# Kernel optimization log

Measured on AMD Instinct MI355X. Metric: run time of the kernel, lower is better.

Reference implementation:

```python
import jax, jax.numpy as jnp
import numpy as np

TEMPERATURE = 0.5
NEG_FILL = -9e15


def setup_inputs() -> dict:
    key = jax.random.key(0)
    k1, k2 = jax.random.split(key)
    B, D = 8192, 128
    z_i = jax.random.normal(k1, (B, D), dtype=jnp.float32)
    z_j = jax.random.normal(k2, (B, D), dtype=jnp.float32)
    return {"z_i": z_i, "z_j": z_j}


def reference(z_i, z_j):
    B = z_i.shape[0]
    N = 2 * B
    z = jnp.concatenate([z_i, z_j], axis=0)              # [2B, D]
    sim = jnp.matmul(z, z.T) / TEMPERATURE               # [2B, 2B]
    # mask out self-similarity on the diagonal
    diag = jnp.eye(N, dtype=bool)
    sim = jnp.where(diag, NEG_FILL, sim)
    # positive pair of row k is row (k+B) mod 2B
    labels = jnp.concatenate([jnp.arange(B, N), jnp.arange(0, B)])
    # CrossEntropyLoss(reduction='sum'): sum_k logsumexp(sim[k]) - sim[k, labels[k]]
    lse = jax.nn.logsumexp(sim, axis=1)                  # [2B]
    pos = sim[jnp.arange(N), labels]                     # [2B]
    loss = jnp.sum(lse - pos)
    return loss / N
```

## Files before the change

### kernel.cpp

```cpp
#include <hip/hip_runtime.h>

#define TEMP    0.5f
#define LOG2E   1.4426950408889634f
#define C2      (LOG2E / TEMP)
#define MSHIFT  160.0f
#define LN2     0.6931471805599453f
#define NROWS   16384
#define BHALF   8192
#define DDIM    128
#define PREPB   2048

typedef __bf16 bf16x8 __attribute__((ext_vector_type(8)));
typedef float  f32x16 __attribute__((ext_vector_type(16)));

__device__ __forceinline__ float fexp2(float x) {
#if __has_builtin(__builtin_amdgcn_exp2f)
  return __builtin_amdgcn_exp2f(x);
#else
  return exp2f(x);
#endif
}

__device__ __forceinline__ unsigned short f2bf(float f) {
  unsigned int u = __float_as_uint(f);
  unsigned int r = (u + 0x7FFFu + ((u >> 16) & 1u)) >> 16;
  return (unsigned short)r;
}


__global__ void k_prep(const float* __restrict__ zi, const float* __restrict__ zj,
                       unsigned short* __restrict__ zbF,
                       float* __restrict__ S, float* __restrict__ Pp) {
  const int t   = blockIdx.x * 256 + threadIdx.x;
  const int row = t >> 5;
  const int k0  = (t & 31) * 4;
  const float* src = (row < BHALF) ? (zi + (size_t)row * DDIM)
                                   : (zj + (size_t)(row - BHALF) * DDIM);
  float4 v = *reinterpret_cast<const float4*>(src + k0);

  const int g = row >> 5, lo = row & 31, khi = k0 >> 3, j0 = k0 & 7;
  ushort4 o;
  o.x = f2bf(v.x); o.y = f2bf(v.y); o.z = f2bf(v.z); o.w = f2bf(v.w);
  *reinterpret_cast<ushort4*>(zbF + (size_t)g * 4096 + khi * 256 + lo * 8 + j0) = o;

  float dot = 0.f;
  if (row < BHALF) {
    float4 w = *reinterpret_cast<const float4*>(zj + (size_t)row * DDIM + k0);
    dot = fmaf(v.x, w.x, fmaf(v.y, w.y, fmaf(v.z, w.z, v.w * w.w)));
  }
#pragma unroll
  for (int m = 32; m >= 1; m >>= 1) dot += __shfl_xor(dot, m, 64);
  __shared__ float red[4];
  if ((threadIdx.x & 63) == 0) red[threadIdx.x >> 6] = dot;
  __syncthreads();
  if (threadIdx.x == 0) Pp[blockIdx.x] = red[0] + red[1] + red[2] + red[3];

  if (t < NROWS) S[t] = 0.f;
}

template <bool MASK>
__device__ __forceinline__ void expAcc(const f32x16& acc, float& sa, float& sb,
                                       int d, int hi) {
#pragma unroll
  for (int r = 0; r < 16; ++r) {
    float e = fexp2(fmaf(acc[r], C2, -MSHIFT));
    if (MASK) {
      const int rloc = (r & 3) + 8 * (r >> 2) + 4 * hi;
      if (rloc == d) e = 0.f;
    }
    if (r & 1) sb += e; else sa += e;
  }
}

__global__ __launch_bounds__(256, 2)
void k_main(const unsigned short* __restrict__ zbF, float* __restrict__ S) {
  const int wave = threadIdx.x >> 6;
  const int lane = threadIdx.x & 63;
  const int lo = lane & 31;
  const int hi = lane >> 5;
  const int rb = blockIdx.x & 31;
  const int cc = blockIdx.x >> 5;
  const int row0w = rb * 512 + wave * 128;

  bf16x8 b[4][8];
#pragma unroll
  for (int rt = 0; rt < 4; ++rt) {
    const unsigned short* bp = zbF + (size_t)((row0w >> 5) + rt) * 4096 + hi * 256 + lo * 8;
#pragma unroll
    for (int ks = 0; ks < 8; ++ks)
      b[rt][ks] = *reinterpret_cast<const bf16x8*>(bp + ks * 512);
  }

  const f32x16 kZ = {};
  float s[4][2];
#pragma unroll
  for (int rt = 0; rt < 4; ++rt) { s[rt][0] = 0.f; s[rt][1] = 0.f; }

  const int c0base = cc * 1024;
  const unsigned short* abase = zbF + (size_t)(c0base >> 5) * 4096 + hi * 256 + lo * 8;

  bf16x8 a[8];
#pragma unroll
  for (int ks = 0; ks < 8; ++ks)
    a[ks] = *reinterpret_cast<const bf16x8*>(abase + ks * 512);

  for (int it = 0; it < 32; ++it) {
    const int c0 = c0base + it * 32;
    const int dr = c0 - row0w;
    const bool dg = (unsigned)dr < 128u;
    const int rtd = dg ? (dr >> 5) : -1;

    f32x16 acc0 = __builtin_amdgcn_mfma_f32_32x32x16_bf16(a[0], b[0][0], kZ, 0, 0, 0);
    f32x16 acc1 = __builtin_amdgcn_mfma_f32_32x32x16_bf16(a[0], b[1][0], kZ, 0, 0, 0);
#pragma unroll
    for (int ks = 1; ks < 8; ++ks) {
      acc0 = __builtin_amdgcn_mfma_f32_32x32x16_bf16(a[ks], b[0][ks], acc0, 0, 0, 0);
      acc1 = __builtin_amdgcn_mfma_f32_32x32x16_bf16(a[ks], b[1][ks], acc1, 0, 0, 0);
    }
    if (!dg) {
      expAcc<false>(acc0, s[0][0], s[0][1], -1, hi);
      expAcc<false>(acc1, s[1][0], s[1][1], -1, hi);
    } else {
      expAcc<true>(acc0, s[0][0], s[0][1], rtd == 0 ? lo : -1, hi);
      expAcc<true>(acc1, s[1][0], s[1][1], rtd == 1 ? lo : -1, hi);
    }

    acc0 = __builtin_amdgcn_mfma_f32_32x32x16_bf16(a[0], b[2][0], kZ, 0, 0, 0);
    acc1 = __builtin_amdgcn_mfma_f32_32x32x16_bf16(a[0], b[3][0], kZ, 0, 0, 0);
#pragma unroll
    for (int ks = 1; ks < 8; ++ks) {
      acc0 = __builtin_amdgcn_mfma_f32_32x32x16_bf16(a[ks], b[2][ks], acc0, 0, 0, 0);
      acc1 = __builtin_amdgcn_mfma_f32_32x32x16_bf16(a[ks], b[3][ks], acc1, 0, 0, 0);
    }

    if (it + 1 < 32) {
      const unsigned short* ap = abase + (size_t)(it + 1) * 4096;
#pragma unroll
      for (int ks = 0; ks < 8; ++ks)
        a[ks] = *reinterpret_cast<const bf16x8*>(ap + ks * 512);
    }

    if (!dg) {
      expAcc<false>(acc0, s[2][0], s[2][1], -1, hi);
      expAcc<false>(acc1, s[3][0], s[3][1], -1, hi);
    } else {
      expAcc<true>(acc0, s[2][0], s[2][1], rtd == 2 ? lo : -1, hi);
      expAcc<true>(acc1, s[3][0], s[3][1], rtd == 3 ? lo : -1, hi);
    }
  }

#pragma unroll
  for (int rt = 0; rt < 4; ++rt) {
    float v = s[rt][0] + s[rt][1];
    v += __shfl_xor(v, 32, 64);
    if (hi == 0) atomicAdd(&S[row0w + rt * 32 + lo], v);
  }
}

__global__ void k_fin(const float* __restrict__ S, const float* __restrict__ Pp,
                      float* __restrict__ out) {
  const int t = threadIdx.x;
  float q = 0.f;
  for (int r = t; r < NROWS; r += 512)
    q += LN2 * (MSHIFT + __log2f(S[r]));
  for (int r = t; r < PREPB; r += 512)
    q -= 4.0f * Pp[r];
  __shared__ float red[512];
  red[t] = q;
  __syncthreads();
  for (int s2 = 256; s2 > 0; s2 >>= 1) {
    if (t < s2) red[t] += red[t + s2];
    __syncthreads();
  }
  if (t == 0) out[0] = red[0] / (float)NROWS;
}

extern "C" void kernel_launch(void* const* d_in, const int* in_sizes, int n_in,
                              void* d_out, int out_size, void* d_ws, size_t ws_size,
                              hipStream_t stream) {
  const float* zi = (const float*)d_in[0];
  const float* zj = (const float*)d_in[1];
  unsigned short* zbF = (unsigned short*)d_ws;
  float* S  = (float*)((char*)d_ws + (size_t)NROWS * DDIM * 2);
  float* Pp = S + NROWS;
  float* out = (float*)d_out;

  hipLaunchKernelGGL(k_prep, dim3(PREPB), dim3(256), 0, stream, zi, zj, zbF, S, Pp);
  hipLaunchKernelGGL(k_main, dim3(512),  dim3(256), 0, stream, zbF, S);
  hipLaunchKernelGGL(k_fin,  dim3(1),    dim3(512), 0, stream, S, Pp, out);
}
```

Measured before the change: 134.6 us.

## Software-pipeline MFMA and exp phases and fuse final reduction into main kernel

The main loop is restructured so the MFMA for the next pair of row tiles is issued before the exp/accumulate of the previous pair, overlapping matrix-core work with transcendental ALU work across iterations. The separate single-block finalize kernel is removed: the last block to finish, detected with an atomic counter and threadfences, performs the log and sum reduction. This removes one kernel launch and its gap, at the cost of extra live accumulator registers and a serialized tail in one block.

```diff
diff --git a/kernel.cpp b/kernel.cpp
--- a/kernel.cpp
+++ b/kernel.cpp
@@ -9,6 +9,7 @@
 #define BHALF   8192
 #define DDIM    128
 #define PREPB   2048
+#define MAINB   512
 
 typedef __bf16 bf16x8 __attribute__((ext_vector_type(8)));
 typedef float  f32x16 __attribute__((ext_vector_type(16)));
@@ -30,7 +31,8 @@
 
 __global__ void k_prep(const float* __restrict__ zi, const float* __restrict__ zj,
                        unsigned short* __restrict__ zbF,
-                       float* __restrict__ S, float* __restrict__ Pp) {
+                       float* __restrict__ S, float* __restrict__ Pp,
+                       unsigned int* __restrict__ Cnt) {
   const int t   = blockIdx.x * 256 + threadIdx.x;
   const int row = t >> 5;
   const int k0  = (t & 31) * 4;
@@ -56,24 +58,49 @@
   if (threadIdx.x == 0) Pp[blockIdx.x] = red[0] + red[1] + red[2] + red[3];
 
   if (t < NROWS) S[t] = 0.f;
-}
-
-template <bool MASK>
-__device__ __forceinline__ void expAcc(const f32x16& acc, float& sa, float& sb,
-                                       int d, int hi) {
+  if (t == 0)    *Cnt = 0u;
+}
+
+__device__ __forceinline__ void loadA(bf16x8 (&a)[8], const unsigned short* ap) {
+#pragma unroll
+  for (int ks = 0; ks < 8; ++ks)
+    a[ks] = *reinterpret_cast<const bf16x8*>(ap + ks * 512);
+}
+
+__device__ __forceinline__ void mfmaPhase(const bf16x8 (&a)[8], const bf16x8 (&b0)[8],
+                                          const bf16x8 (&b1)[8], const f32x16& z,
+                                          f32x16& o0, f32x16& o1) {
+  o0 = __builtin_amdgcn_mfma_f32_32x32x16_bf16(a[0], b0[0], z, 0, 0, 0);
+  o1 = __builtin_amdgcn_mfma_f32_32x32x16_bf16(a[0], b1[0], z, 0, 0, 0);
+#pragma unroll
+  for (int ks = 1; ks < 8; ++ks) {
+    o0 = __builtin_amdgcn_mfma_f32_32x32x16_bf16(a[ks], b0[ks], o0, 0, 0, 0);
+    o1 = __builtin_amdgcn_mfma_f32_32x32x16_bf16(a[ks], b1[ks], o1, 0, 0, 0);
+  }
+}
+
+template <bool MK>
+__device__ __forceinline__ void expPair(const f32x16& A, const f32x16& B,
+                                        float (&sA)[2], float (&sB)[2],
+                                        int dA, int dB, int hi) {
 #pragma unroll
   for (int r = 0; r < 16; ++r) {
-    float e = fexp2(fmaf(acc[r], C2, -MSHIFT));
-    if (MASK) {
+    float eA = fexp2(fmaf(A[r], C2, -MSHIFT));
+    float eB = fexp2(fmaf(B[r], C2, -MSHIFT));
+    if (MK) {
       const int rloc = (r & 3) + 8 * (r >> 2) + 4 * hi;
-      if (rloc == d) e = 0.f;
+      if (rloc == dA) eA = 0.f;
+      if (rloc == dB) eB = 0.f;
     }
-    if (r & 1) sb += e; else sa += e;
+    if (r & 1) { sA[1] += eA; sB[1] += eB; }
+    else       { sA[0] += eA; sB[0] += eB; }
   }
 }
 
 __global__ __launch_bounds__(256, 2)
-void k_main(const unsigned short* __restrict__ zbF, float* __restrict__ S) {
+void k_main(const unsigned short* __restrict__ zbF, float* __restrict__ S,
+            const float* __restrict__ Pp, unsigned int* __restrict__ Cnt,
+            float* __restrict__ out) {
   const int wave = threadIdx.x >> 6;
   const int lane = threadIdx.x & 63;
   const int lo = lane & 31;
@@ -86,9 +113,7 @@
 #pragma unroll
   for (int rt = 0; rt < 4; ++rt) {
     const unsigned short* bp = zbF + (size_t)((row0w >> 5) + rt) * 4096 + hi * 256 + lo * 8;
-#pragma unroll
-    for (int ks = 0; ks < 8; ++ks)
-      b[rt][ks] = *reinterpret_cast<const bf16x8*>(bp + ks * 512);
+    loadA(b[rt], bp);
   }
 
   const f32x16 kZ = {};
@@ -100,53 +125,33 @@
   const unsigned short* abase = zbF + (size_t)(c0base >> 5) * 4096 + hi * 256 + lo * 8;
 
   bf16x8 a[8];
-#pragma unroll
-  for (int ks = 0; ks < 8; ++ks)
-    a[ks] = *reinterpret_cast<const bf16x8*>(abase + ks * 512);
+  loadA(a, abase);
+
+  f32x16 accE0, accE1, accO0, accO1;
+
+  mfmaPhase(a, b[0], b[1], kZ, accE0, accE1);
 
   for (int it = 0; it < 32; ++it) {
-    const int c0 = c0base + it * 32;
-    const int dr = c0 - row0w;
+    const int dr = c0base + it * 32 - row0w;
     const bool dg = (unsigned)dr < 128u;
     const int rtd = dg ? (dr >> 5) : -1;
 
-    f32x16 acc0 = __builtin_amdgcn_mfma_f32_32x32x16_bf16(a[0], b[0][0], kZ, 0, 0, 0);
-    f32x16 acc1 = __builtin_amdgcn_mfma_f32_32x32x16_bf16(a[0], b[1][0], kZ, 0, 0, 0);
-#pragma unroll
-    for (int ks = 1; ks < 8; ++ks) {
-      acc0 = __builtin_amdgcn_mfma_f32_32x32x16_bf16(a[ks], b[0][ks], acc0, 0, 0, 0);
-      acc1 = __builtin_amdgcn_mfma_f32_32x32x16_bf16(a[ks], b[1][ks], acc1, 0, 0, 0);
-    }
-    if (!dg) {
-      expAcc<false>(acc0, s[0][0], s[0][1], -1, hi);
-      expAcc<false>(acc1, s[1][0], s[1][1], -1, hi);
-    } else {
-      expAcc<true>(acc0, s[0][0], s[0][1], rtd == 0 ? lo : -1, hi);
-      expAcc<true>(acc1, s[1][0], s[1][1], rtd == 1 ? lo : -1, hi);
-    }
-
-    acc0 = __builtin_amdgcn_mfma_f32_32x32x16_bf16(a[0], b[2][0], kZ, 0, 0, 0);
-    acc1 = __builtin_amdgcn_mfma_f32_32x32x16_bf16(a[0], b[3][0], kZ, 0, 0, 0);
-#pragma unroll
-    for (int ks = 1; ks < 8; ++ks) {
-      acc0 = __builtin_amdgcn_mfma_f32_32x32x16_bf16(a[ks], b[2][ks], acc0, 0, 0, 0);
-      acc1 = __builtin_amdgcn_mfma_f32_32x32x16_bf16(a[ks], b[3][ks], acc1, 0, 0, 0);
-    }
-
-    if (it + 1 < 32) {
-      const unsigned short* ap = abase + (size_t)(it + 1) * 4096;
-#pragma unroll
-      for (int ks = 0; ks < 8; ++ks)
-        a[ks] = *reinterpret_cast<const bf16x8*>(ap + ks * 512);
-    }
-
-    if (!dg) {
-      expAcc<false>(acc0, s[2][0], s[2][1], -1, hi);
-      expAcc<false>(acc1, s[3][0], s[3][1], -1, hi);
-    } else {
-      expAcc<true>(acc0, s[2][0], s[2][1], rtd == 2 ? lo : -1, hi);
-      expAcc<true>(acc1, s[3][0], s[3][1], rtd == 3 ? lo : -1, hi);
-    }
+    mfmaPhase(a, b[2], b[3], kZ, accO0, accO1);
+    if (it + 1 < 32)
+      loadA(a, abase + (size_t)(it + 1) * 4096);
+
+    if (dg && rtd <= 1)
+      expPair<true >(accE0, accE1, s[0], s[1], rtd == 0 ? lo : -1, rtd == 1 ? lo : -1, hi);
+    else
+      expPair<false>(accE0, accE1, s[0], s[1], -1, -1, hi);
+
+    if (it + 1 < 32)
+      mfmaPhase(a, b[0], b[1], kZ, accE0, accE1);
+
+    if (dg && rtd >= 2)
+      expPair<true >(accO0, accO1, s[2], s[3], rtd == 2 ? lo : -1, rtd == 3 ? lo : -1, hi);
+    else
+      expPair<false>(accO0, accO1, s[2], s[3], -1, -1, hi);
   }
 
 #pragma unroll
@@ -155,20 +160,27 @@
     v += __shfl_xor(v, 32, 64);
     if (hi == 0) atomicAdd(&S[row0w + rt * 32 + lo], v);
   }
-}
-
-__global__ void k_fin(const float* __restrict__ S, const float* __restrict__ Pp,
-                      float* __restrict__ out) {
+
+  __threadfence();
+  __shared__ bool isLast;
+  if (threadIdx.x == 0)
+    isLast = (atomicAdd(Cnt, 1u) == MAINB - 1);
+  __syncthreads();
+  if (!isLast) return;
+  __threadfence();
+
   const int t = threadIdx.x;
   float q = 0.f;
-  for (int r = t; r < NROWS; r += 512)
-    q += LN2 * (MSHIFT + __log2f(S[r]));
-  for (int r = t; r < PREPB; r += 512)
+  for (int r = t; r < NROWS; r += 256) {
+    float sv = __hip_atomic_load(&S[r], __ATOMIC_RELAXED, __HIP_MEMORY_SCOPE_AGENT);
+    q += LN2 * (MSHIFT + __log2f(sv));
+  }
+  for (int r = t; r < PREPB; r += 256)
     q -= 4.0f * Pp[r];
-  __shared__ float red[512];
+  __shared__ float red[256];
   red[t] = q;
   __syncthreads();
-  for (int s2 = 256; s2 > 0; s2 >>= 1) {
+  for (int s2 = 128; s2 > 0; s2 >>= 1) {
     if (t < s2) red[t] += red[t + s2];
     __syncthreads();
   }
@@ -183,9 +195,9 @@
   unsigned short* zbF = (unsigned short*)d_ws;
   float* S  = (float*)((char*)d_ws + (size_t)NROWS * DDIM * 2);
   float* Pp = S + NROWS;
+  unsigned int* Cnt = (unsigned int*)(Pp + PREPB);
   float* out = (float*)d_out;
 
-  hipLaunchKernelGGL(k_prep, dim3(PREPB), dim3(256), 0, stream, zi, zj, zbF, S, Pp);
-  hipLaunchKernelGGL(k_main, dim3(512),  dim3(256), 0, stream, zbF, S);
-  hipLaunchKernelGGL(k_fin,  dim3(1),    dim3(512), 0, stream, S, Pp, out);
-}
+  hipLaunchKernelGGL(k_prep, dim3(PREPB), dim3(256), 0, stream, zi, zj, zbF, S, Pp, Cnt);
+  hipLaunchKernelGGL(k_main, dim3(MAINB), dim3(256), 0, stream, zbF, S, Pp, Cnt, out);
+}
```

Result: slower. 173.1 us (+28.6%).
